# Kernel tuning notes

Measured on AMD Instinct MI355X. Metric: run time of the kernel, lower is better.

## Reference

```python
import jax, jax.numpy as jnp
import numpy as np

# ---- constants derived from module config ----
DEG_HIST = np.array([0., 12000., 20000., 13000., 4000., 1000.])
AVG_DEG_LOG = float((np.log(np.arange(len(DEG_HIST)) + 1.0) * DEG_HIST).sum() / DEG_HIST.sum())
N_NODES, N_EDGES, N_GRAPHS = 50000, 150000, 2000
D, E_D, TOWERS, F_OUT, N_LAYERS = 75, 50, 5, 15, 4
EPS = 1e-5


def setup_inputs() -> dict:
    key = jax.random.key(0)
    ks = jax.random.split(key, 16)
    g = lambda k, shape, s=0.05: (jax.random.normal(k, shape, jnp.float32) * s)
    return {
        'x': jax.random.randint(ks[0], (N_NODES,), 0, 21),
        'edge_index': jax.random.randint(ks[1], (2, N_EDGES), 0, N_NODES),
        'edge_attr': jax.random.randint(ks[2], (N_EDGES,), 0, 4),
        'batch': jnp.sort(jax.random.randint(ks[3], (N_NODES,), 0, N_GRAPHS)),
        'node_emb': g(ks[4], (21, D), 1.0),
        'edge_emb': g(ks[5], (4, E_D), 1.0),
        'We': g(ks[6], (N_LAYERS, E_D, D)),
        'be': jnp.zeros((N_LAYERS, D), jnp.float32),
        'Wpre': g(ks[7], (N_LAYERS, TOWERS, 3 * D, D)),
        'bpre': jnp.zeros((N_LAYERS, TOWERS, D), jnp.float32),
        'Wpost': g(ks[8], (N_LAYERS, TOWERS, 13 * D, F_OUT)),
        'bpost': jnp.zeros((N_LAYERS, TOWERS, F_OUT), jnp.float32),
        'Wlin': g(ks[9], (N_LAYERS, D, D)),
        'blin': jnp.zeros((N_LAYERS, D), jnp.float32),
        'gamma': jnp.ones((N_LAYERS, D), jnp.float32),
        'beta': jnp.zeros((N_LAYERS, D), jnp.float32),
        'W1': g(ks[10], (D, 50)), 'b1': jnp.zeros((50,), jnp.float32),
        'W2': g(ks[11], (50, 25)), 'b2': jnp.zeros((25,), jnp.float32),
        'W3': g(ks[12], (25, 1)), 'b3': jnp.zeros((1,), jnp.float32),
    }


def _pna_layer(x, src, dst, e_emb, We, be, Wpre, bpre, Wpost, bpost, Wlin, blin):
    # edge encoder (shared across towers)
    e = e_emb @ We + be                                        # [E, D]
    h = jnp.concatenate([x[dst], x[src], e], axis=-1)          # [E, 3D] = (x_i, x_j, e)
    m = jnp.einsum('ec,tcf->etf', h, Wpre) + bpre              # [E, T, D] per-tower pre_nn
    # multi-aggregator scatter (mean / min / max / std) onto target nodes
    deg = jax.ops.segment_sum(jnp.ones((src.shape[0],), x.dtype), dst, num_segments=N_NODES)
    denom = jnp.maximum(deg, 1.0)[:, None, None]
    mean = jax.ops.segment_sum(m, dst, num_segments=N_NODES) / denom
    mean_sq = jax.ops.segment_sum(m * m, dst, num_segments=N_NODES) / denom
    std = jnp.sqrt(jax.nn.relu(mean_sq - mean * mean) + 1e-5)
    has = (deg > 0)[:, None, None]
    mn = jnp.where(has, jax.ops.segment_min(m, dst, num_segments=N_NODES), 0.0)
    mx = jnp.where(has, jax.ops.segment_max(m, dst, num_segments=N_NODES), 0.0)
    agg = jnp.concatenate([mean, mn, mx, std], axis=-1)        # [N, T, 4D]
    # degree scalers: identity / amplification / attenuation
    amp = jnp.log(jnp.maximum(deg, 1.0) + 1.0)[:, None, None] / AVG_DEG_LOG
    out = jnp.concatenate([agg, agg * amp, agg / amp], axis=-1)  # [N, T, 12D]
    xt = jnp.broadcast_to(x[:, None, :], (x.shape[0], TOWERS, D))  # divide_input=False
    out = jnp.concatenate([xt, out], axis=-1)                   # [N, T, 13D]
    out = jnp.einsum('ntc,tcf->ntf', out, Wpost) + bpost        # [N, T, F_OUT] per-tower post_nn
    out = out.reshape(x.shape[0], TOWERS * F_OUT)               # [N, D]
    return out @ Wlin + blin


def _bn(x, gamma, beta):
    mu = x.mean(0)
    var = ((x - mu) ** 2).mean(0)  # biased, training-mode batch stats
    return gamma * (x - mu) / jnp.sqrt(var + EPS) + beta


def reference(x, edge_index, edge_attr, batch, node_emb, edge_emb, We, be, Wpre, bpre,
              Wpost, bpost, Wlin, blin, gamma, beta, W1, b1, W2, b2, W3, b3):
    src, dst = edge_index[0], edge_index[1]
    h = node_emb[x]                 # [N, 75]
    ea = edge_emb[edge_attr]        # [E, 50]
    for l in range(N_LAYERS):
        h = jax.nn.relu(_bn(_pna_layer(h, src, dst, ea, We[l], be[l], Wpre[l], bpre[l],
                                       Wpost[l], bpost[l], Wlin[l], blin[l]),
                            gamma[l], beta[l]))
    pooled = jax.ops.segment_sum(h, batch, num_segments=N_GRAPHS)  # global_add_pool
    z = jax.nn.relu(pooled @ W1 + b1)
    z = jax.nn.relu(z @ W2 + b2)
    return z @ W3 + b3  # [N_GRAPHS, 1]
```

## Files before the change

kernel.cpp:

```cpp
#include <hip/hip_runtime.h>
#include <math.h>

#define NN 50000
#define NE 150000
#define NG 2000
#define NL 4
#define AVG_DEG_LOG 1.1308269950720915f

typedef __attribute__((ext_vector_type(8))) short bf8_t;
typedef __attribute__((ext_vector_type(4))) float f4_t;

__device__ inline unsigned short f2bf(float x) {
  union { float f; unsigned int u; } v; v.f = x;
  unsigned int r = (v.u + 0x7FFFu + ((v.u >> 16) & 1u)) >> 16;
  return (unsigned short)r;
}
__device__ inline float bflo(unsigned int u) { union { unsigned int u; float f; } v; v.u = u << 16; return v.f; }
__device__ inline float bfhi(unsigned int u) { union { unsigned int u; float f; } v; v.u = u & 0xFFFF0000u; return v.f; }

__device__ inline bf8_t ldfrag(const float* __restrict__ zrow, int k0, int bn,
                               const float* __restrict__ musig,
                               const float* __restrict__ gm, const float* __restrict__ bt) {
  bf8_t r;
  #pragma unroll
  for (int j = 0; j < 8; ++j) {
    int k = k0 + j;
    float x = 0.0f;
    if (k < 75) {
      x = zrow[k];
      if (bn) x = fmaxf(gm[k] * (x - musig[k]) * musig[75 + k] + bt[k], 0.0f);
    }
    r[j] = (short)f2bf(x);
  }
  return r;
}

__global__ void k_deg(const int* __restrict__ dst, int* __restrict__ deg) {
  int e = blockIdx.x * 256 + threadIdx.x;
  if (e < NE) atomicAdd(&deg[dst[e]], 1);
}

__global__ __launch_bounds__(1024) void k_scan(const int* __restrict__ deg, int* __restrict__ off) {
  __shared__ int wsum[16];
  __shared__ int wpre[16];
  __shared__ int carry_s;
  int tid = threadIdx.x, lane = tid & 63, wv = tid >> 6;
  if (tid == 0) carry_s = 0;
  __syncthreads();
  for (int base = 0; base < NN; base += 1024) {
    int i = base + tid;
    int v = (i < NN) ? deg[i] : 0;
    int incl = v;
    #pragma unroll
    for (int d = 1; d < 64; d <<= 1) { int t = __shfl_up(incl, d); if (lane >= d) incl += t; }
    if (lane == 63) wsum[wv] = incl;
    __syncthreads();
    if (wv == 0) {
      int s = (lane < 16) ? wsum[lane] : 0;
      int sc = s;
      #pragma unroll
      for (int d = 1; d < 16; d <<= 1) { int t = __shfl_up(sc, d); if (lane >= d) sc += t; }
      if (lane < 16) wpre[lane] = sc - s;
    }
    __syncthreads();
    int carry = carry_s;
    int excl = carry + wpre[wv] + incl - v;
    if (i < NN) off[i] = excl;
    __syncthreads();
    if (tid == 1023) carry_s = excl + v;
    __syncthreads();
  }
  if (tid == 0) off[NN] = carry_s;
}

__global__ void k_amp(const int* __restrict__ deg, const int* __restrict__ off,
                      float* __restrict__ amp, float* __restrict__ invamp,
                      float* __restrict__ gate, int* __restrict__ cursor) {
  int n = blockIdx.x * 256 + threadIdx.x;
  if (n < NN) {
    int d0 = deg[n];
    int d = d0 < 1 ? 1 : d0;
    float a = logf((float)d + 1.0f) / AVG_DEG_LOG;
    amp[n] = a; invamp[n] = 1.0f / a;
    gate[n] = (d0 > 0) ? 1.0f : 0.0f;
    cursor[n] = off[n];
  }
}

__global__ void k_fill(const int* __restrict__ src, const int* __restrict__ dst,
                       const int* __restrict__ attr, int* __restrict__ cursor,
                       unsigned int* __restrict__ cpack) {
  int e = blockIdx.x * 256 + threadIdx.x;
  if (e < NE) {
    int d = dst[e];
    int p = atomicAdd(&cursor[d], 1);
    cpack[p] = (unsigned int)src[e] | ((unsigned int)attr[e] << 16);
  }
}

__global__ void k_embed(const int* __restrict__ x, const float* __restrict__ emb, float* __restrict__ Zf) {
  int i = blockIdx.x * 256 + threadIdx.x;
  if (i < NN * 76) {
    int n = i / 76, c = i - (i / 76) * 76;
    Zf[i] = (c < 75) ? emb[x[n] * 75 + c] : 0.0f;
  }
}

__global__ void k_wxlin(const float* __restrict__ Wpost, const float* __restrict__ Wlin, float* __restrict__ WXlin) {
  int l = blockIdx.x;
  for (int idx = threadIdx.x; idx < 5625; idx += 256) {
    int k = idx / 75, j = idx - (idx / 75) * 75;
    float s = 0.0f;
    for (int o = 0; o < 75; ++o) {
      int t = o / 15, jj = o - t * 15;
      s += Wpost[((l * 5 + t) * 975 + k) * 15 + jj] * Wlin[l * 5625 + o * 75 + j];
    }
    WXlin[l * 5625 + idx] = s;
  }
}

__global__ void k_zb(const float* __restrict__ bpost, const float* __restrict__ blin,
                     const float* __restrict__ Wlin, float* __restrict__ zb) {
  int l = blockIdx.x, j = threadIdx.x;
  if (j < 75) {
    float s = blin[l * 75 + j];
    for (int o = 0; o < 75; ++o) s += bpost[l * 75 + o] * Wlin[l * 5625 + o * 75 + j];
    zb[l * 75 + j] = s;
  }
}

__global__ void k_wy(const float* __restrict__ Wpre, const float* __restrict__ bpre,
                     const float* __restrict__ Wpost, float* __restrict__ WY, float* __restrict__ bY) {
  __shared__ float wsum[1125];
  int b = blockIdx.x;
  int l = b / 15, rr = b - l * 15, t = rr / 3, s = rr - (rr / 3) * 3;
  int tid = threadIdx.x;
  for (int it = tid; it < 1125; it += 256) {
    int f = it / 15, jj = it - (it / 15) * 15;
    float acc = 0.0f;
    #pragma unroll
    for (int agg = 0; agg < 3; ++agg)
      acc += Wpost[((l * 5 + t) * 975 + 75 + s * 300 + agg * 75 + f) * 15 + jj];
    wsum[f * 15 + jj] = acc;
  }
  __syncthreads();
  for (int it = tid; it < 1140; it += 256) {
    int k = it / 15, jj = it - (it / 15) * 15;
    float acc = 0.0f;
    if (k < 75) {
      for (int f = 0; f < 75; ++f)
        acc += Wpre[((l * 5 + t) * 225 + k) * 75 + f] * wsum[f * 15 + jj];
      WY[((l * 3 + s) * 75 + k) * 75 + t * 15 + jj] = acc;
    } else {
      for (int f = 0; f < 75; ++f)
        acc += bpre[l * 375 + t * 75 + f] * wsum[f * 15 + jj];
      bY[(l * 3 + s) * 75 + t * 15 + jj] = acc;
    }
  }
}

__global__ void k_packAll(const float* __restrict__ Wpre, const float* __restrict__ WXlin,
                          const float* __restrict__ WY, const float* __restrict__ Wlin,
                          unsigned short* __restrict__ B1Ts, unsigned short* __restrict__ WXYT,
                          unsigned short* __restrict__ WlinT) {
  const int S1 = 4 * 384 * 96;
  const int S2 = S1 + 4 * 320 * 96;
  const int S3 = S2 + 4 * 80 * 96;
  int idx = blockIdx.x * 256 + threadIdx.x;
  if (idx < S1) {
    int l = idx / (384 * 96); int rem = idx - l * (384 * 96);
    int c = rem / 96, k = rem - (rem / 96) * 96;
    float v = 0.0f;
    if (c < 375 && k < 75) {
      int t = c / 75, f = c - t * 75;
      v = Wpre[((l * 5 + t) * 225 + 75 + k) * 75 + f];
    }
    B1Ts[idx] = f2bf(v);
  } else if (idx < S2) {
    int m = idx - S1;
    int l = m / (320 * 96); int rem = m - l * (320 * 96);
    int c = rem / 96, k = rem - (rem / 96) * 96;
    float v = 0.0f;
    if (k < 75) {
      if (c < 80) {
        if (c < 75) v = WXlin[l * 5625 + k * 75 + c];
      } else {
        int g = c - 80; int t = g / 48; int r = g - t * 48; int s = r / 16; int jj = r - s * 16;
        if (jj < 15) v = WY[((l * 3 + s) * 75 + k) * 75 + t * 15 + jj];
      }
    }
    WXYT[m] = f2bf(v);
  } else if (idx < S3) {
    int m = idx - S2;
    int l = m / (80 * 96); int rem = m - l * (80 * 96);
    int j = rem / 96, k = rem - (rem / 96) * 96;
    float v = (j < 75 && k < 75) ? Wlin[l * 5625 + k * 75 + j] : 0.0f;
    WlinT[m] = f2bf(v);
  }
}

__global__ void k_packWcomb(const float* __restrict__ Wpost, unsigned short* __restrict__ WcombT) {
  int idx = blockIdx.x * 256 + threadIdx.x;
  if (idx >= 4 * 5 * 48 * 320) return;
  int l = idx / (5 * 48 * 320); int rem = idx - l * (5 * 48 * 320);
  int t = rem / (48 * 320); rem -= t * (48 * 320);
  int j = rem / 320, k = rem - (rem / 320) * 320;
  float v = 0.0f;
  if (j < 45 && k < 300) {
    int s = j / 15, jj = j - s * 15;
    int f = k >> 2, agg = k & 3;
    v = Wpost[((l * 5 + t) * 975 + 75 + s * 300 + agg * 75 + f) * 15 + jj];
  }
  WcombT[idx] = f2bf(v);
}

__global__ void k_etab(const float* __restrict__ edge_emb, const float* __restrict__ We,
                       const float* __restrict__ be, const float* __restrict__ Wpre,
                       float* __restrict__ etab) {
  __shared__ float ev[75];
  int l = blockIdx.x >> 2, a = blockIdx.x & 3;
  int tid = threadIdx.x;
  if (tid < 75) {
    float acc = be[l * 75 + tid];
    for (int k = 0; k < 50; ++k) acc += edge_emb[a * 50 + k] * We[(l * 50 + k) * 75 + tid];
    ev[tid] = acc;
  }
  __syncthreads();
  for (int tf = tid; tf < 384; tf += 256) {
    float acc = 0.0f;
    if (tf < 375) {
      int t = tf / 75, f = tf - t * 75;
      for (int d = 0; d < 75; ++d) acc += ev[d] * Wpre[((l * 5 + t) * 225 + 150 + d) * 75 + f];
    }
    etab[(l * 4 + a) * 384 + tf] = acc;
  }
}

__global__ __launch_bounds__(256) void k_gemm1(const float* __restrict__ Zf,
                                               const float* __restrict__ bnsum,
                                               const float* __restrict__ gm, const float* __restrict__ bt,
                                               int bn,
                                               const unsigned short* __restrict__ B1Ts_l,
                                               unsigned short* __restrict__ Hsrc,
                                               unsigned short* __restrict__ hb) {
  __shared__ float ms_s[150];
  int tid = threadIdx.x;
  if (tid < 75) {
    float mu = bnsum[tid] * (1.0f / NN);
    float var = fmaxf(bnsum[75 + tid] * (1.0f / NN) - mu * mu, 0.0f);
    ms_s[tid] = mu;
    ms_s[75 + tid] = 1.0f / sqrtf(var + 1e-5f);
  }
  __syncthreads();
  int w = tid >> 6, lane = tid & 63;
  int l15 = lane & 15, l4 = lane >> 4;
  int m0 = blockIdx.x * 64 + w * 16;
  int mA = m0 + l15; if (mA >= NN) mA = NN - 1;
  const float* zrow = Zf + (size_t)mA * 76;
  bf8_t a0 = ldfrag(zrow, l4 * 8, bn, ms_s, gm, bt);
  bf8_t a1 = ldfrag(zrow, 32 + l4 * 8, bn, ms_s, gm, bt);
  bf8_t a2 = ldfrag(zrow, 64 + l4 * 8, bn, ms_s, gm, bt);
  {
    unsigned short* hrow = hb + (size_t)mA * 96 + l4 * 8;
    *(bf8_t*)(hrow) = a0;
    *(bf8_t*)(hrow + 32) = a1;
    *(bf8_t*)(hrow + 64) = a2;
  }
  for (int nf = 0; nf < 24; ++nf) {
    int c = nf * 16 + l15;
    const unsigned short* bp = B1Ts_l + (size_t)c * 96 + l4 * 8;
    f4_t acc = {0.f, 0.f, 0.f, 0.f};
    acc = __builtin_amdgcn_mfma_f32_16x16x32_bf16(a0, *(const bf8_t*)(bp), acc, 0, 0, 0);
    acc = __builtin_amdgcn_mfma_f32_16x16x32_bf16(a1, *(const bf8_t*)(bp + 32), acc, 0, 0, 0);
    acc = __builtin_amdgcn_mfma_f32_16x16x32_bf16(a2, *(const bf8_t*)(bp + 64), acc, 0, 0, 0);
    #pragma unroll
    for (int i = 0; i < 4; ++i) {
      int m = m0 + l4 * 4 + i;
      if (m < NN) Hsrc[(size_t)m * 384 + c] = f2bf(acc[i]);
    }
  }
}

__global__ __launch_bounds__(256) void k_gather(const unsigned short* __restrict__ Hsrc,
                                                const int* __restrict__ off,
                                                const unsigned int* __restrict__ cpack,
                                                const float* __restrict__ etab_l,
                                                unsigned short* __restrict__ A) {
  __shared__ float et_s[1536];
  int tid = threadIdx.x, w = tid >> 6, lane = tid & 63;
  for (int it = tid; it < 1536; it += 256) {
    int aa = it / 384, c = it - aa * 384;
    et_s[aa * 384 + (c ^ (((c >> 3) & 7) << 2))] = etab_l[it];
  }
  __syncthreads();
  int g = blockIdx.x * 4 + w;
  int e0 = off[g], e1 = off[g + 1];
  unsigned short* arow = A + (size_t)g * 1600;
  if (lane < 47) {
    int c0 = lane * 8;
    int cs = c0 ^ (((c0 >> 3) & 7) << 2);
    float s8[8], q8[8], mn8[8], mx8[8];
    #pragma unroll
    for (int j = 0; j < 8; ++j) {
      s8[j] = 0.0f; q8[j] = 0.0f;
      mn8[j] = 3.402823466e+38f; mx8[j] = -3.402823466e+38f;
    }
    auto acc8 = [&](bf8_t hv, unsigned int aa) {
      union { bf8_t v; unsigned int u[4]; } cv; cv.v = hv;
      f4_t ea = *(const f4_t*)&et_s[aa * 384 + cs];
      f4_t eb = *(const f4_t*)&et_s[aa * 384 + (cs ^ 4)];
      float vv[8], ee[8];
      #pragma unroll
      for (int j = 0; j < 4; ++j) {
        vv[2 * j] = bflo(cv.u[j]); vv[2 * j + 1] = bfhi(cv.u[j]);
        ee[j] = ea[j]; ee[4 + j] = eb[j];
      }
      #pragma unroll
      for (int j = 0; j < 8; ++j) {
        float q = vv[j] + ee[j];
        s8[j] += q;
        q8[j] = fmaf(q, q, q8[j]);
        mn8[j] = fminf(mn8[j], q);
        mx8[j] = fmaxf(mx8[j], q);
      }
    };
    for (int e = e0; e < e1; ) {
      int m = e1 - e;
      unsigned int pk0 = cpack[e];
      unsigned int pk1 = cpack[m > 1 ? e + 1 : e];
      unsigned int pk2 = cpack[m > 2 ? e + 2 : e];
      unsigned int pk3 = cpack[m > 3 ? e + 3 : e];
      bf8_t h0 = *((const bf8_t*)(Hsrc + (size_t)(pk0 & 0xFFFFu) * 384) + lane);
      bf8_t h1 = *((const bf8_t*)(Hsrc + (size_t)(pk1 & 0xFFFFu) * 384) + lane);
      bf8_t h2 = *((const bf8_t*)(Hsrc + (size_t)(pk2 & 0xFFFFu) * 384) + lane);
      bf8_t h3 = *((const bf8_t*)(Hsrc + (size_t)(pk3 & 0xFFFFu) * 384) + lane);
      acc8(h0, pk0 >> 16);
      if (m > 1) acc8(h1, pk1 >> 16);
      if (m > 2) acc8(h2, pk2 >> 16);
      if (m > 3) acc8(h3, pk3 >> 16);
      e += (m < 4) ? m : 4;
    }
    int d = e1 - e0;
    float inv = (d > 0) ? (1.0f / (float)d) : 0.0f;
    #pragma unroll
    for (int j = 0; j < 8; ++j) {
      int c = c0 + j;
      if (c < 375) {
        float mean, mnv, mxv, sd;
        if (d > 0) {
          float mu = s8[j] * inv;
          mean = mu; mnv = mn8[j]; mxv = mx8[j];
          sd = sqrtf(fmaxf(q8[j] * inv - mu * mu, 0.0f) + 1e-5f);
        } else { mean = 0.0f; mnv = 0.0f; mxv = 0.0f; sd = 0.0031622776601683794f; }
        int t = c / 75, f = c - (c / 75) * 75;
        uint2 pkv;
        pkv.x = (unsigned int)f2bf(mean) | ((unsigned int)f2bf(mnv) << 16);
        pkv.y = (unsigned int)f2bf(mxv) | ((unsigned int)f2bf(sd) << 16);
        *(uint2*)&arow[t * 320 + f * 4] = pkv;
      }
    }
  } else {
    uint2 z; z.x = 0u; z.y = 0u;
    for (int k = lane - 47; k < 25; k += 17) {
      int t = k / 5, q = k - (k / 5) * 5;
      *(uint2*)&arow[t * 320 + 300 + q * 4] = z;
    }
  }
}

__global__ __launch_bounds__(256) void k_ptower(const unsigned short* __restrict__ A,
                                                const unsigned short* __restrict__ hb,
                                                const unsigned short* __restrict__ WcombT_l,
                                                const unsigned short* __restrict__ WXYT_l,
                                                const float* __restrict__ ampv,
                                                const float* __restrict__ invampv,
                                                const float* __restrict__ gatev,
                                                const float* __restrict__ bY_l,
                                                unsigned short* __restrict__ Cbg) {
  __shared__ __align__(16) float Out_s[64 * 99];
  __shared__ float amp_s[64], inv_s[64], gate_s[64];
  __shared__ float bY_s[45];
  int tid = threadIdx.x;
  int w = tid >> 6, lane = tid & 63;
  int l15 = lane & 15, l4 = lane >> 4;
  int t = blockIdx.y;
  int m0 = blockIdx.x * 64;

  for (int r = tid; r < 64; r += 256) {
    int m = m0 + r; if (m >= NN) m = NN - 1;
    amp_s[r] = ampv[m]; inv_s[r] = invampv[m]; gate_s[r] = gatev[m];
  }
  if (tid < 45) {
    int s = tid / 15, jj = tid - s * 15;
    bY_s[tid] = bY_l[s * 75 + t * 15 + jj];
  }
  int mh = m0 + w * 16 + l15; if (mh >= NN) mh = NN - 1;
  const unsigned short* arow = A + (size_t)mh * 1600 + t * 320 + l4 * 8;
  bf8_t af[10];
  #pragma unroll
  for (int ks = 0; ks < 10; ++ks) af[ks] = *(const bf8_t*)(arow + ks * 32);
  const unsigned short* hrow = hb + (size_t)mh * 96 + l4 * 8;
  bf8_t hb0 = *(const bf8_t*)(hrow);
  bf8_t hb1 = *(const bf8_t*)(hrow + 32);
  bf8_t hb2 = *(const bf8_t*)(hrow + 64);

  f4_t tw0 = {0.f,0.f,0.f,0.f}, tw1 = {0.f,0.f,0.f,0.f}, tw2 = {0.f,0.f,0.f,0.f};
  const unsigned short* wp0 = WcombT_l + (size_t)(t * 48 + l15) * 320 + l4 * 8;
  const unsigned short* wp1 = WcombT_l + (size_t)(t * 48 + 16 + l15) * 320 + l4 * 8;
  const unsigned short* wp2 = WcombT_l + (size_t)(t * 48 + 32 + l15) * 320 + l4 * 8;
  #pragma unroll
  for (int ks = 0; ks < 10; ++ks) {
    tw0 = __builtin_amdgcn_mfma_f32_16x16x32_bf16(af[ks], *(const bf8_t*)(wp0 + ks * 32), tw0, 0, 0, 0);
    tw1 = __builtin_amdgcn_mfma_f32_16x16x32_bf16(af[ks], *(const bf8_t*)(wp1 + ks * 32), tw1, 0, 0, 0);
    tw2 = __builtin_amdgcn_mfma_f32_16x16x32_bf16(af[ks], *(const bf8_t*)(wp2 + ks * 32), tw2, 0, 0, 0);
  }
  f4_t yv[3];
  #pragma unroll
  for (int s = 0; s < 3; ++s) {
    const unsigned short* bp = WXYT_l + (size_t)(80 + t * 48 + s * 16 + l15) * 96 + l4 * 8;
    f4_t acc = {0.f, 0.f, 0.f, 0.f};
    acc = __builtin_amdgcn_mfma_f32_16x16x32_bf16(hb0, *(const bf8_t*)(bp), acc, 0, 0, 0);
    acc = __builtin_amdgcn_mfma_f32_16x16x32_bf16(hb1, *(const bf8_t*)(bp + 32), acc, 0, 0, 0);
    acc = __builtin_amdgcn_mfma_f32_16x16x32_bf16(hb2, *(const bf8_t*)(bp + 64), acc, 0, 0, 0);
    yv[s] = acc;
  }
  #pragma unroll
  for (int i = 0; i < 4; ++i) {
    int rb = w * 16 + l4 * 4 + i;
    Out_s[rb * 99 + l15] = tw0[i];
    Out_s[rb * 99 + 16 + l15] = tw1[i];
    Out_s[rb * 99 + 32 + l15] = tw2[i];
    Out_s[rb * 99 + 48 + l15] = yv[0][i];
    Out_s[rb * 99 + 64 + l15] = yv[1][i];
    Out_s[rb * 99 + 80 + l15] = yv[2][i];
  }
  __syncthreads();
  for (int item = tid; item < 1024; item += 256) {
    int r = item >> 4, jj = item & 15;
    int m = m0 + r;
    if (jj < 15 && m < NN) {
      const float* ob = &Out_s[r * 99];
      float gt = gate_s[r];
      float v1 = ob[jj]      + gt * (ob[48 + jj] + bY_s[jj]);
      float v2 = ob[15 + jj] + gt * (ob[64 + jj] + bY_s[15 + jj]);
      float v3 = ob[30 + jj] + gt * (ob[80 + jj] + bY_s[30 + jj]);
      Cbg[(size_t)m * 96 + t * 15 + jj] = f2bf(v1 + amp_s[r] * v2 + inv_s[r] * v3);
    }
  }
}

__global__ __launch_bounds__(256) void k_lin(const unsigned short* __restrict__ Cbg,
                                             const unsigned short* __restrict__ hb,
                                             const unsigned short* __restrict__ WXYT_l,
                                             const unsigned short* __restrict__ WlinT_l,
                                             const float* __restrict__ zb_l,
                                             float* __restrict__ Zf,
                                             float* __restrict__ bnsum) {
  __shared__ float bnred[152];
  int tid = threadIdx.x;
  int w = tid >> 6, lane = tid & 63;
  int l15 = lane & 15, l4 = lane >> 4;
  int m0 = blockIdx.x * 64;
  if (tid < 152) bnred[tid] = 0.0f;
  __syncthreads();
  int mh = m0 + w * 16 + l15; if (mh >= NN) mh = NN - 1;
  const unsigned short* hrow = hb + (size_t)mh * 96 + l4 * 8;
  bf8_t hb0 = *(const bf8_t*)(hrow);
  bf8_t hb1 = *(const bf8_t*)(hrow + 32);
  bf8_t hb2 = *(const bf8_t*)(hrow + 64);
  const unsigned short* crow = Cbg + (size_t)mh * 96 + l4 * 8;
  bf8_t cf0 = *(const bf8_t*)(crow);
  bf8_t cf1 = *(const bf8_t*)(crow + 32);
  bf8_t cf2 = *(const bf8_t*)(crow + 64);
  #pragma unroll
  for (int fx = 0; fx < 5; ++fx) {
    int cc = fx * 16 + l15;
    const unsigned short* xp = WXYT_l + (size_t)cc * 96 + l4 * 8;
    f4_t x0 = {0.f, 0.f, 0.f, 0.f};
    x0 = __builtin_amdgcn_mfma_f32_16x16x32_bf16(hb0, *(const bf8_t*)(xp), x0, 0, 0, 0);
    x0 = __builtin_amdgcn_mfma_f32_16x16x32_bf16(hb1, *(const bf8_t*)(xp + 32), x0, 0, 0, 0);
    x0 = __builtin_amdgcn_mfma_f32_16x16x32_bf16(hb2, *(const bf8_t*)(xp + 64), x0, 0, 0, 0);
    const unsigned short* bp = WlinT_l + (size_t)cc * 96 + l4 * 8;
    f4_t acc = {0.f, 0.f, 0.f, 0.f};
    acc = __builtin_amdgcn_mfma_f32_16x16x32_bf16(cf0, *(const bf8_t*)(bp), acc, 0, 0, 0);
    acc = __builtin_amdgcn_mfma_f32_16x16x32_bf16(cf1, *(const bf8_t*)(bp + 32), acc, 0, 0, 0);
    acc = __builtin_amdgcn_mfma_f32_16x16x32_bf16(cf2, *(const bf8_t*)(bp + 64), acc, 0, 0, 0);
    if (cc < 75) {
      float s = 0.0f, q = 0.0f;
      #pragma unroll
      for (int i = 0; i < 4; ++i) {
        int m = m0 + w * 16 + l4 * 4 + i;
        if (m < NN) {
          float z = acc[i] + x0[i] + zb_l[cc];
          Zf[(size_t)m * 76 + cc] = z;
          s += z; q = fmaf(z, z, q);
        }
      }
      s += __shfl_xor(s, 16); q += __shfl_xor(q, 16);
      s += __shfl_xor(s, 32); q += __shfl_xor(q, 32);
      if (l4 == 0) {
        atomicAdd(&bnred[cc], s);
        atomicAdd(&bnred[76 + cc], q);
      }
    }
  }
  __syncthreads();
  if (tid < 75) atomicAdd(&bnsum[tid], bnred[tid]);
  else if (tid >= 76 && tid < 151) atomicAdd(&bnsum[tid - 1], bnred[tid]);
}

__global__ __launch_bounds__(128) void k_pool_mlp(const float* __restrict__ Zf, const int* __restrict__ batch,
                                                  const float* __restrict__ bnsum,
                                                  const float* __restrict__ gm, const float* __restrict__ bt,
                                                  const float* __restrict__ W1, const float* __restrict__ b1,
                                                  const float* __restrict__ W2, const float* __restrict__ b2,
                                                  const float* __restrict__ W3, const float* __restrict__ b3,
                                                  float* __restrict__ out) {
  __shared__ float pooled[75];
  __shared__ float ms_s[150];
  __shared__ float z1[50];
  __shared__ float z2[25];
  __shared__ int se[2];
  int g = blockIdx.x, tid = threadIdx.x;
  if (tid < 2) {
    int target = g + tid;
    int lo = 0, hi = NN;
    while (lo < hi) { int mid = (lo + hi) >> 1; if (batch[mid] < target) lo = mid + 1; else hi = mid; }
    se[tid] = lo;
  }
  if (tid < 75) {
    float mu = bnsum[tid] * (1.0f / NN);
    float var = fmaxf(bnsum[75 + tid] * (1.0f / NN) - mu * mu, 0.0f);
    ms_s[tid] = mu;
    ms_s[75 + tid] = 1.0f / sqrtf(var + 1e-5f);
  }
  __syncthreads();
  int s = se[0], e = se[1];
  if (tid < 75) {
    float mu = ms_s[tid], sig = ms_s[75 + tid], gmc = gm[tid], btc = bt[tid];
    float acc = 0.0f;
    for (int r = s; r < e; ++r)
      acc += fmaxf(gmc * (Zf[(size_t)r * 76 + tid] - mu) * sig + btc, 0.0f);
    pooled[tid] = acc;
  }
  __syncthreads();
  if (tid < 50) {
    float acc = b1[tid];
    for (int c = 0; c < 75; ++c) acc += pooled[c] * W1[c * 50 + tid];
    z1[tid] = fmaxf(acc, 0.0f);
  }
  __syncthreads();
  if (tid < 25) {
    float acc = b2[tid];
    for (int c = 0; c < 50; ++c) acc += z1[c] * W2[c * 25 + tid];
    z2[tid] = fmaxf(acc, 0.0f);
  }
  __syncthreads();
  if (tid == 0) {
    float acc = b3[0];
    for (int c = 0; c < 25; ++c) acc += z2[c] * W3[c];
    out[g] = acc;
  }
}

extern "C" void kernel_launch(void* const* d_in, const int* in_sizes, int n_in,
                              void* d_out, int out_size, void* d_ws, size_t ws_size,
                              hipStream_t stream) {
  const int* x = (const int*)d_in[0];
  const int* ei = (const int*)d_in[1];
  const int* eattr = (const int*)d_in[2];
  const int* batch = (const int*)d_in[3];
  const float* node_emb = (const float*)d_in[4];
  const float* edge_emb = (const float*)d_in[5];
  const float* We = (const float*)d_in[6];
  const float* be = (const float*)d_in[7];
  const float* Wpre = (const float*)d_in[8];
  const float* bpre = (const float*)d_in[9];
  const float* Wpost = (const float*)d_in[10];
  const float* bpost = (const float*)d_in[11];
  const float* Wlin = (const float*)d_in[12];
  const float* blin = (const float*)d_in[13];
  const float* gamma = (const float*)d_in[14];
  const float* beta = (const float*)d_in[15];
  const float* W1 = (const float*)d_in[16];
  const float* b1 = (const float*)d_in[17];
  const float* W2 = (const float*)d_in[18];
  const float* b2 = (const float*)d_in[19];
  const float* W3 = (const float*)d_in[20];
  const float* b3 = (const float*)d_in[21];
  float* out = (float*)d_out;

  const int* src = ei;
  const int* dst = ei + NE;

  char* p = (char*)d_ws;
  auto alloc = [&](size_t bytes) { char* r = p; p += (bytes + 255) & ~(size_t)255; return r; };
  int* deg     = (int*)alloc((size_t)NN * 4);
  int* off     = (int*)alloc((size_t)(NN + 1) * 4);
  int* cursor  = (int*)alloc((size_t)NN * 4);
  unsigned int* cpack = (unsigned int*)alloc((size_t)NE * 4);
  float* amp    = (float*)alloc((size_t)NN * 4);
  float* invamp = (float*)alloc((size_t)NN * 4);
  float* gate   = (float*)alloc((size_t)NN * 4);
  float* Zf            = (float*)alloc((size_t)NN * 76 * 4 + 256);
  unsigned short* Hsrc = (unsigned short*)alloc((size_t)NN * 384 * 2 + 256);
  unsigned short* hbv  = (unsigned short*)alloc((size_t)NN * 96 * 2 + 256);
  unsigned short* Cbg  = (unsigned short*)alloc((size_t)NN * 96 * 2 + 256);
  unsigned short* Abuf = (unsigned short*)alloc((size_t)NN * 1600 * 2 + 256);
  unsigned short* B1Ts   = (unsigned short*)alloc((size_t)4 * 384 * 96 * 2);
  unsigned short* WXYT   = (unsigned short*)alloc((size_t)4 * 320 * 96 * 2);
  unsigned short* WlinT  = (unsigned short*)alloc((size_t)4 * 80 * 96 * 2);
  unsigned short* WcombT = (unsigned short*)alloc((size_t)4 * 5 * 48 * 320 * 2);
  float* WXlin = (float*)alloc((size_t)4 * 5625 * 4);
  float* WY    = (float*)alloc((size_t)4 * 3 * 75 * 75 * 4);
  float* bY    = (float*)alloc((size_t)4 * 3 * 75 * 4);
  float* zb    = (float*)alloc((size_t)4 * 75 * 4);
  float* etab  = (float*)alloc((size_t)4 * 4 * 384 * 4);
  float* bnsum  = (float*)alloc((size_t)152 * 4);

  hipMemsetAsync(deg, 0, (size_t)NN * 4, stream);
  k_deg<<<(NE + 255) / 256, 256, 0, stream>>>(dst, deg);
  k_scan<<<1, 1024, 0, stream>>>(deg, off);
  k_amp<<<(NN + 255) / 256, 256, 0, stream>>>(deg, off, amp, invamp, gate, cursor);
  k_fill<<<(NE + 255) / 256, 256, 0, stream>>>(src, dst, eattr, cursor, cpack);
  k_embed<<<(NN * 76 + 255) / 256, 256, 0, stream>>>(x, node_emb, Zf);
  k_wxlin<<<4, 256, 0, stream>>>(Wpost, Wlin, WXlin);
  k_wy<<<60, 256, 0, stream>>>(Wpre, bpre, Wpost, WY, bY);
  k_zb<<<4, 128, 0, stream>>>(bpost, blin, Wlin, zb);
  {
    int tot = 4 * 384 * 96 + 4 * 320 * 96 + 4 * 80 * 96;
    k_packAll<<<(tot + 255) / 256, 256, 0, stream>>>(Wpre, WXlin, WY, Wlin, B1Ts, WXYT, WlinT);
  }
  k_packWcomb<<<(4 * 5 * 48 * 320 + 255) / 256, 256, 0, stream>>>(Wpost, WcombT);
  k_etab<<<16, 256, 0, stream>>>(edge_emb, We, be, Wpre, etab);

  for (int l = 0; l < NL; ++l) {
    const float* gm = gamma + (l > 0 ? (l - 1) * 75 : 0);
    const float* bt = beta + (l > 0 ? (l - 1) * 75 : 0);
    int bn = (l > 0) ? 1 : 0;
    k_gemm1<<<(NN + 63) / 64, 256, 0, stream>>>(Zf, bnsum, gm, bt, bn,
                                                B1Ts + (size_t)l * 384 * 96, Hsrc, hbv);
    hipMemsetAsync(bnsum, 0, 152 * 4, stream);
    k_gather<<<NN / 4, 256, 0, stream>>>(Hsrc, off, cpack, etab + (size_t)l * 4 * 384, Abuf);
    {
      dim3 gp((NN + 63) / 64, 5);
      k_ptower<<<gp, 256, 0, stream>>>(Abuf, hbv,
                                       WcombT + (size_t)l * 5 * 48 * 320,
                                       WXYT + (size_t)l * 320 * 96,
                                       amp, invamp, gate,
                                       bY + (size_t)l * 225, Cbg);
    }
    k_lin<<<(NN + 63) / 64, 256, 0, stream>>>(Cbg, hbv,
                                              WXYT + (size_t)l * 320 * 96,
                                              WlinT + (size_t)l * 80 * 96,
                                              zb + l * 75, Zf, bnsum);
  }
  k_pool_mlp<<<NG, 128, 0, stream>>>(Zf, batch, bnsum, gamma + 225, beta + 225,
                                     W1, b1, W2, b2, W3, b3, out);
}
```

Measured before the change: 1.277 ms.

## Pad per-tower feature stride to 80 and make aggregate buffer tower-major

Each tower's 75 pre-features are padded to 80 columns (400 per row) in Hsrc, B1Ts and etab. With that padding every gather lane covers exactly one tower slice, so each lane can write its mean/min/max/std block as full 16-byte stores into a tower-major A buffer, replacing scattered 8-byte stores and the separate zero-fill path. k_gemm1 stages its output tile in LDS and writes it to global memory as coalesced uint4 rows, and k_ptower now uses the tower index as the fast grid dimension and reads contiguous tower-major A. Per-layer BN sums get separate buffers cleared by one upfront memset, which removes the memset inside the layer loop. The cost is slightly more memory traffic for the padding and 52KB of LDS per block in gemm1, which may lower occupancy.

```diff
diff --git a/kernel.cpp b/kernel.cpp
--- a/kernel.cpp
+++ b/kernel.cpp
@@ -163,18 +163,17 @@
                           const float* __restrict__ WY, const float* __restrict__ Wlin,
                           unsigned short* __restrict__ B1Ts, unsigned short* __restrict__ WXYT,
                           unsigned short* __restrict__ WlinT) {
-  const int S1 = 4 * 384 * 96;
+  const int S1 = 4 * 400 * 96;
   const int S2 = S1 + 4 * 320 * 96;
   const int S3 = S2 + 4 * 80 * 96;
   int idx = blockIdx.x * 256 + threadIdx.x;
   if (idx < S1) {
-    int l = idx / (384 * 96); int rem = idx - l * (384 * 96);
+    int l = idx / (400 * 96); int rem = idx - l * (400 * 96);
     int c = rem / 96, k = rem - (rem / 96) * 96;
+    int t = c / 80, f = c - t * 80;
     float v = 0.0f;
-    if (c < 375 && k < 75) {
-      int t = c / 75, f = c - t * 75;
+    if (f < 75 && k < 75)
       v = Wpre[((l * 5 + t) * 225 + 75 + k) * 75 + f];
-    }
     B1Ts[idx] = f2bf(v);
   } else if (idx < S2) {
     int m = idx - S1;
@@ -205,10 +204,10 @@
   int l = idx / (5 * 48 * 320); int rem = idx - l * (5 * 48 * 320);
   int t = rem / (48 * 320); rem -= t * (48 * 320);
   int j = rem / 320, k = rem - (rem / 320) * 320;
+  int f = k >> 2, agg = k & 3;
   float v = 0.0f;
-  if (j < 45 && k < 300) {
+  if (j < 45 && f < 75) {
     int s = j / 15, jj = j - s * 15;
-    int f = k >> 2, agg = k & 3;
     v = Wpost[((l * 5 + t) * 975 + 75 + s * 300 + agg * 75 + f) * 15 + jj];
   }
   WcombT[idx] = f2bf(v);
@@ -226,13 +225,13 @@
     ev[tid] = acc;
   }
   __syncthreads();
-  for (int tf = tid; tf < 384; tf += 256) {
+  for (int c = tid; c < 400; c += 256) {
+    int t = c / 80, f = c - t * 80;
     float acc = 0.0f;
-    if (tf < 375) {
-      int t = tf / 75, f = tf - t * 75;
+    if (f < 75) {
       for (int d = 0; d < 75; ++d) acc += ev[d] * Wpre[((l * 5 + t) * 225 + 150 + d) * 75 + f];
     }
-    etab[(l * 4 + a) * 384 + tf] = acc;
+    etab[(l * 4 + a) * 400 + c] = acc;
   }
 }
 
@@ -244,6 +243,7 @@
                                                unsigned short* __restrict__ Hsrc,
                                                unsigned short* __restrict__ hb) {
   __shared__ float ms_s[150];
+  __shared__ __align__(16) unsigned short H_s[64 * 408];
   int tid = threadIdx.x;
   if (tid < 75) {
     float mu = bnsum[tid] * (1.0f / NN);
@@ -254,8 +254,8 @@
   __syncthreads();
   int w = tid >> 6, lane = tid & 63;
   int l15 = lane & 15, l4 = lane >> 4;
-  int m0 = blockIdx.x * 64 + w * 16;
-  int mA = m0 + l15; if (mA >= NN) mA = NN - 1;
+  int m0 = blockIdx.x * 64;
+  int mA = m0 + w * 16 + l15; if (mA >= NN) mA = NN - 1;
   const float* zrow = Zf + (size_t)mA * 76;
   bf8_t a0 = ldfrag(zrow, l4 * 8, bn, ms_s, gm, bt);
   bf8_t a1 = ldfrag(zrow, 32 + l4 * 8, bn, ms_s, gm, bt);
@@ -266,7 +266,7 @@
     *(bf8_t*)(hrow + 32) = a1;
     *(bf8_t*)(hrow + 64) = a2;
   }
-  for (int nf = 0; nf < 24; ++nf) {
+  for (int nf = 0; nf < 25; ++nf) {
     int c = nf * 16 + l15;
     const unsigned short* bp = B1Ts_l + (size_t)c * 96 + l4 * 8;
     f4_t acc = {0.f, 0.f, 0.f, 0.f};
@@ -274,10 +274,15 @@
     acc = __builtin_amdgcn_mfma_f32_16x16x32_bf16(a1, *(const bf8_t*)(bp + 32), acc, 0, 0, 0);
     acc = __builtin_amdgcn_mfma_f32_16x16x32_bf16(a2, *(const bf8_t*)(bp + 64), acc, 0, 0, 0);
     #pragma unroll
-    for (int i = 0; i < 4; ++i) {
-      int m = m0 + l4 * 4 + i;
-      if (m < NN) Hsrc[(size_t)m * 384 + c] = f2bf(acc[i]);
-    }
+    for (int i = 0; i < 4; ++i)
+      H_s[(w * 16 + l4 * 4 + i) * 408 + c] = f2bf(acc[i]);
+  }
+  __syncthreads();
+  for (int idx = tid; idx < 3200; idx += 256) {
+    int row = idx / 50, q = idx - row * 50;
+    int m = m0 + row;
+    if (m < NN)
+      *(uint4*)&Hsrc[(size_t)m * 400 + q * 8] = *(const uint4*)&H_s[row * 408 + q * 8];
   }
 }
 
@@ -286,86 +291,78 @@
                                                 const unsigned int* __restrict__ cpack,
                                                 const float* __restrict__ etab_l,
                                                 unsigned short* __restrict__ A) {
-  __shared__ float et_s[1536];
+  __shared__ float et_s[1600];
   int tid = threadIdx.x, w = tid >> 6, lane = tid & 63;
-  for (int it = tid; it < 1536; it += 256) {
-    int aa = it / 384, c = it - aa * 384;
-    et_s[aa * 384 + (c ^ (((c >> 3) & 7) << 2))] = etab_l[it];
-  }
-  __syncthreads();
+  for (int it = tid; it < 1600; it += 256) {
+    int aa = it / 400, c = it - aa * 400;
+    et_s[aa * 400 + (c ^ (((c >> 3) & 7) << 2))] = etab_l[it];
+  }
+  __syncthreads();
+  if (lane >= 50) return;
   int g = blockIdx.x * 4 + w;
   int e0 = off[g], e1 = off[g + 1];
-  unsigned short* arow = A + (size_t)g * 1600;
-  if (lane < 47) {
-    int c0 = lane * 8;
-    int cs = c0 ^ (((c0 >> 3) & 7) << 2);
-    float s8[8], q8[8], mn8[8], mx8[8];
+  int c0 = lane * 8;
+  int cs = c0 ^ (((c0 >> 3) & 7) << 2);
+  int t = lane / 10;
+  int f0 = c0 - t * 80;
+  const bf8_t* hbase = (const bf8_t*)Hsrc + lane;
+  float s8[8], q8[8], mn8[8], mx8[8];
+  #pragma unroll
+  for (int j = 0; j < 8; ++j) {
+    s8[j] = 0.0f; q8[j] = 0.0f;
+    mn8[j] = 3.402823466e+38f; mx8[j] = -3.402823466e+38f;
+  }
+  auto acc8 = [&](bf8_t hv, unsigned int aa) {
+    union { bf8_t v; unsigned int u[4]; } cv; cv.v = hv;
+    f4_t ea = *(const f4_t*)&et_s[aa * 400 + cs];
+    f4_t eb = *(const f4_t*)&et_s[aa * 400 + (cs ^ 4)];
     #pragma unroll
     for (int j = 0; j < 8; ++j) {
-      s8[j] = 0.0f; q8[j] = 0.0f;
-      mn8[j] = 3.402823466e+38f; mx8[j] = -3.402823466e+38f;
-    }
-    auto acc8 = [&](bf8_t hv, unsigned int aa) {
-      union { bf8_t v; unsigned int u[4]; } cv; cv.v = hv;
-      f4_t ea = *(const f4_t*)&et_s[aa * 384 + cs];
-      f4_t eb = *(const f4_t*)&et_s[aa * 384 + (cs ^ 4)];
-      float vv[8], ee[8];
-      #pragma unroll
-      for (int j = 0; j < 4; ++j) {
-        vv[2 * j] = bflo(cv.u[j]); vv[2 * j + 1] = bfhi(cv.u[j]);
-        ee[j] = ea[j]; ee[4 + j] = eb[j];
-      }
-      #pragma unroll
-      for (int j = 0; j < 8; ++j) {
-        float q = vv[j] + ee[j];
-        s8[j] += q;
-        q8[j] = fmaf(q, q, q8[j]);
-        mn8[j] = fminf(mn8[j], q);
-        mx8[j] = fmaxf(mx8[j], q);
-      }
-    };
-    for (int e = e0; e < e1; ) {
-      int m = e1 - e;
-      unsigned int pk0 = cpack[e];
-      unsigned int pk1 = cpack[m > 1 ? e + 1 : e];
-      unsigned int pk2 = cpack[m > 2 ? e + 2 : e];
-      unsigned int pk3 = cpack[m > 3 ? e + 3 : e];
-      bf8_t h0 = *((const bf8_t*)(Hsrc + (size_t)(pk0 & 0xFFFFu) * 384) + lane);
-      bf8_t h1 = *((const bf8_t*)(Hsrc + (size_t)(pk1 & 0xFFFFu) * 384) + lane);
-      bf8_t h2 = *((const bf8_t*)(Hsrc + (size_t)(pk2 & 0xFFFFu) * 384) + lane);
-      bf8_t h3 = *((const bf8_t*)(Hsrc + (size_t)(pk3 & 0xFFFFu) * 384) + lane);
-      acc8(h0, pk0 >> 16);
-      if (m > 1) acc8(h1, pk1 >> 16);
-      if (m > 2) acc8(h2, pk2 >> 16);
-      if (m > 3) acc8(h3, pk3 >> 16);
-      e += (m < 4) ? m : 4;
-    }
-    int d = e1 - e0;
-    float inv = (d > 0) ? (1.0f / (float)d) : 0.0f;
+      float h = (j & 1) ? bfhi(cv.u[j >> 1]) : bflo(cv.u[j >> 1]);
+      float e = (j < 4) ? ea[j] : eb[j - 4];
+      float q = h + e;
+      s8[j] += q;
+      q8[j] = fmaf(q, q, q8[j]);
+      mn8[j] = fminf(mn8[j], q);
+      mx8[j] = fmaxf(mx8[j], q);
+    }
+  };
+  for (int e = e0; e < e1; ) {
+    int m = e1 - e;
+    unsigned int pk0 = cpack[e];
+    unsigned int pk1 = cpack[m > 1 ? e + 1 : e];
+    unsigned int pk2 = cpack[m > 2 ? e + 2 : e];
+    unsigned int pk3 = cpack[m > 3 ? e + 3 : e];
+    bf8_t h0 = hbase[(pk0 & 0xFFFFu) * 50];
+    bf8_t h1 = hbase[(pk1 & 0xFFFFu) * 50];
+    bf8_t h2 = hbase[(pk2 & 0xFFFFu) * 50];
+    bf8_t h3 = hbase[(pk3 & 0xFFFFu) * 50];
+    acc8(h0, pk0 >> 16);
+    if (m > 1) acc8(h1, pk1 >> 16);
+    if (m > 2) acc8(h2, pk2 >> 16);
+    if (m > 3) acc8(h3, pk3 >> 16);
+    e += (m < 4) ? m : 4;
+  }
+  int d = e1 - e0;
+  unsigned short* abase = A + ((size_t)t * NN + g) * 320 + f0 * 4;
+  uint4 pk[4];
+  unsigned int* pw = (unsigned int*)pk;
+  if (d > 0) {
+    float inv = 1.0f / (float)d;
     #pragma unroll
     for (int j = 0; j < 8; ++j) {
-      int c = c0 + j;
-      if (c < 375) {
-        float mean, mnv, mxv, sd;
-        if (d > 0) {
-          float mu = s8[j] * inv;
-          mean = mu; mnv = mn8[j]; mxv = mx8[j];
-          sd = sqrtf(fmaxf(q8[j] * inv - mu * mu, 0.0f) + 1e-5f);
-        } else { mean = 0.0f; mnv = 0.0f; mxv = 0.0f; sd = 0.0031622776601683794f; }
-        int t = c / 75, f = c - (c / 75) * 75;
-        uint2 pkv;
-        pkv.x = (unsigned int)f2bf(mean) | ((unsigned int)f2bf(mnv) << 16);
-        pkv.y = (unsigned int)f2bf(mxv) | ((unsigned int)f2bf(sd) << 16);
-        *(uint2*)&arow[t * 320 + f * 4] = pkv;
-      }
+      float mu = s8[j] * inv;
+      float sd = sqrtf(fmaxf(q8[j] * inv - mu * mu, 0.0f) + 1e-5f);
+      pw[j * 2]     = (unsigned int)f2bf(mu) | ((unsigned int)f2bf(mn8[j]) << 16);
+      pw[j * 2 + 1] = (unsigned int)f2bf(mx8[j]) | ((unsigned int)f2bf(sd) << 16);
     }
   } else {
-    uint2 z; z.x = 0u; z.y = 0u;
-    for (int k = lane - 47; k < 25; k += 17) {
-      int t = k / 5, q = k - (k / 5) * 5;
-      *(uint2*)&arow[t * 320 + 300 + q * 4] = z;
-    }
-  }
+    unsigned int zsd = (unsigned int)f2bf(0.0031622776601683794f) << 16;
+    #pragma unroll
+    for (int j = 0; j < 8; ++j) { pw[j * 2] = 0u; pw[j * 2 + 1] = zsd; }
+  }
+  #pragma unroll
+  for (int jj = 0; jj < 4; ++jj) *(uint4*)(abase + jj * 8) = pk[jj];
 }
 
 __global__ __launch_bounds__(256) void k_ptower(const unsigned short* __restrict__ A,
@@ -383,8 +380,8 @@
   int tid = threadIdx.x;
   int w = tid >> 6, lane = tid & 63;
   int l15 = lane & 15, l4 = lane >> 4;
-  int t = blockIdx.y;
-  int m0 = blockIdx.x * 64;
+  int t = blockIdx.x;
+  int m0 = blockIdx.y * 64;
 
   for (int r = tid; r < 64; r += 256) {
     int m = m0 + r; if (m >= NN) m = NN - 1;
@@ -395,7 +392,7 @@
     bY_s[tid] = bY_l[s * 75 + t * 15 + jj];
   }
   int mh = m0 + w * 16 + l15; if (mh >= NN) mh = NN - 1;
-  const unsigned short* arow = A + (size_t)mh * 1600 + t * 320 + l4 * 8;
+  const unsigned short* arow = A + ((size_t)t * NN + mh) * 320 + l4 * 8;
   bf8_t af[10];
   #pragma unroll
   for (int ks = 0; ks < 10; ++ks) af[ks] = *(const bf8_t*)(arow + ks * 32);
@@ -603,11 +600,11 @@
   float* invamp = (float*)alloc((size_t)NN * 4);
   float* gate   = (float*)alloc((size_t)NN * 4);
   float* Zf            = (float*)alloc((size_t)NN * 76 * 4 + 256);
-  unsigned short* Hsrc = (unsigned short*)alloc((size_t)NN * 384 * 2 + 256);
+  unsigned short* Hsrc = (unsigned short*)alloc((size_t)NN * 400 * 2 + 256);
   unsigned short* hbv  = (unsigned short*)alloc((size_t)NN * 96 * 2 + 256);
   unsigned short* Cbg  = (unsigned short*)alloc((size_t)NN * 96 * 2 + 256);
-  unsigned short* Abuf = (unsigned short*)alloc((size_t)NN * 1600 * 2 + 256);
-  unsigned short* B1Ts   = (unsigned short*)alloc((size_t)4 * 384 * 96 * 2);
+  unsigned short* Abuf = (unsigned short*)alloc((size_t)5 * NN * 320 * 2 + 256);
+  unsigned short* B1Ts   = (unsigned short*)alloc((size_t)4 * 400 * 96 * 2);
   unsigned short* WXYT   = (unsigned short*)alloc((size_t)4 * 320 * 96 * 2);
   unsigned short* WlinT  = (unsigned short*)alloc((size_t)4 * 80 * 96 * 2);
   unsigned short* WcombT = (unsigned short*)alloc((size_t)4 * 5 * 48 * 320 * 2);
@@ -615,10 +612,11 @@
   float* WY    = (float*)alloc((size_t)4 * 3 * 75 * 75 * 4);
   float* bY    = (float*)alloc((size_t)4 * 3 * 75 * 4);
   float* zb    = (float*)alloc((size_t)4 * 75 * 4);
-  float* etab  = (float*)alloc((size_t)4 * 4 * 384 * 4);
-  float* bnsum  = (float*)alloc((size_t)152 * 4);
+  float* etab  = (float*)alloc((size_t)4 * 4 * 400 * 4);
+  float* bnsum  = (float*)alloc((size_t)4 * 152 * 4);
 
   hipMemsetAsync(deg, 0, (size_t)NN * 4, stream);
+  hipMemsetAsync(bnsum, 0, (size_t)4 * 152 * 4, stream);
   k_deg<<<(NE + 255) / 256, 256, 0, stream>>>(dst, deg);
   k_scan<<<1, 1024, 0, stream>>>(deg, off);
   k_amp<<<(NN + 255) / 256, 256, 0, stream>>>(deg, off, amp, invamp, gate, cursor);
@@ -628,7 +626,7 @@
   k_wy<<<60, 256, 0, stream>>>(Wpre, bpre, Wpost, WY, bY);
   k_zb<<<4, 128, 0, stream>>>(bpost, blin, Wlin, zb);
   {
-    int tot = 4 * 384 * 96 + 4 * 320 * 96 + 4 * 80 * 96;
+    int tot = 4 * 400 * 96 + 4 * 320 * 96 + 4 * 80 * 96;
     k_packAll<<<(tot + 255) / 256, 256, 0, stream>>>(Wpre, WXlin, WY, Wlin, B1Ts, WXYT, WlinT);
   }
   k_packWcomb<<<(4 * 5 * 48 * 320 + 255) / 256, 256, 0, stream>>>(Wpost, WcombT);
@@ -638,12 +636,13 @@
     const float* gm = gamma + (l > 0 ? (l - 1) * 75 : 0);
     const float* bt = beta + (l > 0 ? (l - 1) * 75 : 0);
     int bn = (l > 0) ? 1 : 0;
-    k_gemm1<<<(NN + 63) / 64, 256, 0, stream>>>(Zf, bnsum, gm, bt, bn,
-                                                B1Ts + (size_t)l * 384 * 96, Hsrc, hbv);
-    hipMemsetAsync(bnsum, 0, 152 * 4, stream);
-    k_gather<<<NN / 4, 256, 0, stream>>>(Hsrc, off, cpack, etab + (size_t)l * 4 * 384, Abuf);
+    const float* bnsum_prev = bnsum + (size_t)(l > 0 ? l - 1 : 0) * 152;
+    float* bnsum_cur = bnsum + (size_t)l * 152;
+    k_gemm1<<<(NN + 63) / 64, 256, 0, stream>>>(Zf, bnsum_prev, gm, bt, bn,
+                                                B1Ts + (size_t)l * 400 * 96, Hsrc, hbv);
+    k_gather<<<NN / 4, 256, 0, stream>>>(Hsrc, off, cpack, etab + (size_t)l * 4 * 400, Abuf);
     {
-      dim3 gp((NN + 63) / 64, 5);
+      dim3 gp(5, (NN + 63) / 64);
       k_ptower<<<gp, 256, 0, stream>>>(Abuf, hbv,
                                        WcombT + (size_t)l * 5 * 48 * 320,
                                        WXYT + (size_t)l * 320 * 96,
@@ -653,8 +652,9 @@
     k_lin<<<(NN + 63) / 64, 256, 0, stream>>>(Cbg, hbv,
                                               WXYT + (size_t)l * 320 * 96,
                                               WlinT + (size_t)l * 80 * 96,
-                                              zb + l * 75, Zf, bnsum);
-  }
-  k_pool_mlp<<<NG, 128, 0, stream>>>(Zf, batch, bnsum, gamma + 225, beta + 225,
+                                              zb + l * 75, Zf, bnsum_cur);
+  }
+  k_pool_mlp<<<NG, 128, 0, stream>>>(Zf, batch, bnsum + (size_t)(NL - 1) * 152,
+                                     gamma + 225, beta + 225,
                                      W1, b1, W2, b2, W3, b3, out);
 }
```

After: 1.200 ms (median of 4 runs). 6.0% less time.
